# Kernel optimization log

Measured on AMD Instinct MI355X. Metric: run time of the kernel, lower is better.

## Reference

```python
import jax, jax.numpy as jnp
import numpy as np

B, L, DS, DP = 4, 384, 384, 128
NEAR_BAND = 4
LN_EPS = 1e-5


def setup_inputs():
    key = jax.random.key(0)
    k = jax.random.split(key, 16)
    return {
        "seq_repr": jax.random.normal(k[0], (B, L, DS), jnp.float32),
        "pair_repr": jax.random.normal(k[1], (B, L, L, DP), jnp.float32),
        "ln_s_g": 1.0 + 0.1 * jax.random.normal(k[2], (DS,), jnp.float32),
        "ln_s_b": 0.1 * jax.random.normal(k[3], (DS,), jnp.float32),
        "ln_z_g": 1.0 + 0.1 * jax.random.normal(k[4], (DP,), jnp.float32),
        "ln_z_b": 0.1 * jax.random.normal(k[5], (DP,), jnp.float32),
        "W_seq": jax.random.normal(k[6], (DS, DS), jnp.float32) / np.sqrt(DS).astype(np.float32),
        "W_pair": jax.random.normal(k[7], (DP, DP), jnp.float32) / np.sqrt(DP).astype(np.float32),
        "W_gs": 0.02 * jax.random.normal(k[8], (2 * DS, DS), jnp.float32),
        "b_gs": jnp.ones((DS,), jnp.float32),
        "W_gz": 0.02 * jax.random.normal(k[9], (2 * DP, DP), jnp.float32),
        "b_gz": jnp.ones((DP,), jnp.float32),
        "W1": jax.random.normal(k[10], (DS + 2 * DP, 64), jnp.float32) / np.sqrt(DS + 2 * DP).astype(np.float32),
        "b1": 0.01 * jax.random.normal(k[11], (64,), jnp.float32),
        "W2": jax.random.normal(k[12], (64, 1), jnp.float32) / 8.0,
        "b2": jnp.zeros((1,), jnp.float32),
        "chain_id": jax.random.randint(k[13], (B, L), 0, 2, jnp.int32),
        "mask": jax.random.randint(k[14], (B, L), 0, 2, jnp.int32).astype(jnp.bool_),
    }


def _layernorm(x, g, b):
    mu = jnp.mean(x, axis=-1, keepdims=True)
    var = jnp.mean(jnp.square(x - mu), axis=-1, keepdims=True)
    return (x - mu) * jax.lax.rsqrt(var + LN_EPS) * g + b


def _masked_mean(x, m, axes):
    num = jnp.sum(x * m, axis=axes)
    den = jnp.clip(jnp.sum(m, axis=axes), 1e-6, None)  # mask has trailing dim 1 -> den broadcasts
    return num / den


def _masked_max(x, m, axis):
    v = jnp.max(jnp.where(m > 0, x, -jnp.inf), axis=axis)
    return jnp.where(jnp.isinf(v), jnp.zeros_like(v), v)


def reference(seq_repr, pair_repr, ln_s_g, ln_s_b, ln_z_g, ln_z_b, W_seq, W_pair,
              W_gs, b_gs, W_gz, b_gz, W1, b1, W2, b2, chain_id, mask):
    # sequence branch: LN -> Linear -> masked mean/max over L -> gated blend
    s = _layernorm(seq_repr, ln_s_g, ln_s_b) @ W_seq          # [B,L,DS]
    m = mask.astype(s.dtype)[..., None]                        # [B,L,1]
    s_mean = _masked_mean(s, m, 1)                             # [B,DS]
    s_max = _masked_max(s, m, 1)                               # [B,DS]
    gate_s = jax.nn.sigmoid(jnp.concatenate([s_max, s_mean], -1) @ W_gs + b_gs)
    s_feat = s_mean + gate_s * (s_max - s_mean)

    # pair branch: symmetrize, zero diagonal, LN -> Linear
    p = 0.5 * (pair_repr + jnp.swapaxes(pair_repr, 1, 2))      # [B,L,L,DP]
    eye = jnp.eye(L, dtype=p.dtype)[None, :, :, None]
    p = p * (1.0 - eye)
    p = _layernorm(p, ln_z_g, ln_z_b) @ W_pair

    pm = (mask[:, :, None] & mask[:, None, :])[..., None].astype(p.dtype)   # [B,L,L,1]
    same = (chain_id[:, :, None] == chain_id[:, None, :])[..., None]
    intra = pm * same.astype(p.dtype)
    inter = pm * (~same).astype(p.dtype)

    inter_mean = _masked_mean(p, inter, (1, 2))                # [B,DP]
    row_den = jnp.clip(jnp.sum(inter, axis=2), 1e-6, None)     # [B,L,1]
    row_mean = jnp.sum(p * inter, axis=2) / row_den            # [B,L,DP]
    inter_peak = jnp.max(row_mean, axis=1)                     # [B,DP]
    gate_z = jax.nn.sigmoid(jnp.concatenate([inter_peak, inter_mean], -1) @ W_gz + b_gz)
    inter_feat = inter_mean + gate_z * (inter_peak - inter_mean)

    idx = jnp.arange(L)
    band = (jnp.abs(idx[:, None] - idx[None, :]) <= NEAR_BAND)[None, :, :, None].astype(p.dtype)
    intra_compact = _masked_mean(p, intra * band, (1, 2))      # [B,DP]

    feat = jnp.concatenate([s_feat, inter_feat, intra_compact], -1)  # [B, DS+2*DP]
    h = jax.nn.relu(feat @ W1 + b1)
    prob = jax.nn.sigmoid(h @ W2 + b2)[..., 0]                 # [B]
    return prob
```

## Files before the change

kernel.cpp:

```cpp
#include <hip/hip_runtime.h>
#include <hip/hip_bf16.h>
#include <math.h>

#define B_  4
#define L_  384
#define DS_ 384
#define DP_ 128
#define NB_ 4
#define FEAT_ (DS_ + 2*DP_)
#define LN_EPS_ 1e-5f
#define T_ 16
#define NT_ (L_ / T_)
#define NTP_ (NT_ * (NT_ + 1) / 2)
#define NCH_ 8
#define CHROWS_ (L_ / NCH_)

__device__ __forceinline__ void atomAddF(float* p, float v) {
    unsafeAtomicAdd(p, v);
}

__global__ __launch_bounds__(256) void k_mask(const void* __restrict__ mask_raw,
                                              int* __restrict__ maskN, int n) {
    const unsigned int* dw = (const unsigned int*)mask_raw;
    int tid = threadIdx.x;
    int local_int = 1, local_flt = 1;
    for (int i = tid; i < n / 4; i += blockDim.x) {
        unsigned int v = dw[i];
        if (v != 0u && v != 1u) local_int = 0;
        if (v != 0u && v != 0x3F800000u) local_flt = 0;
    }
    int all_int = __syncthreads_and(local_int);
    int all_flt = __syncthreads_and(local_flt);
    if (all_int) {
        for (int i = tid; i < n; i += blockDim.x) maskN[i] = (dw[i] != 0u) ? 1 : 0;
    } else if (all_flt) {
        const float* f = (const float*)mask_raw;
        for (int i = tid; i < n; i += blockDim.x) maskN[i] = (f[i] != 0.0f) ? 1 : 0;
    } else {
        const unsigned char* by = (const unsigned char*)mask_raw;
        for (int i = tid; i < n; i += blockDim.x) maskN[i] = by[i] ? 1 : 0;
    }
}

__global__ __launch_bounds__(256) void k_pair_tiles(
    const float* __restrict__ pair, const float* __restrict__ gz,
    const float* __restrict__ bz, const int* __restrict__ chain,
    const int* __restrict__ maskN,
    float* __restrict__ rs_inter, float* __restrict__ rs_intra,
    float* __restrict__ den_inter, float* __restrict__ den_intra) {
    extern __shared__ float lds[];
    float* smJI = lds;
    float* smJA = smJI + 4 * 16 * 128;
    float* smDJI = smJA + 4 * 16 * 128;
    float* smDJA = smDJI + 64;
    int* s_mi = (int*)(smDJA + 64);
    int* s_ci = s_mi + 16;
    int* s_mj = s_ci + 16;
    int* s_cj = s_mj + 16;

    const int b = blockIdx.x / NTP_;
    int t = blockIdx.x % NTP_;
    int ta = 0;
    while (t >= NT_ - ta) { t -= NT_ - ta; ta++; }
    const int tb = ta + t;
    const int i0 = ta * T_, j0 = tb * T_;
    const float fac = (ta == tb) ? 0.5f : 1.0f;

    const int tid = threadIdx.x;
    const int wave = tid >> 6, lane = tid & 63;
    const int ch2 = lane * 2;

    for (int idx = tid; idx < 4 * 16 * 128; idx += 256) { smJI[idx] = 0.f; smJA[idx] = 0.f; }
    if (tid < 64) { smDJI[tid] = 0.f; smDJA[tid] = 0.f; }
    if (tid < 16) {
        s_mi[tid] = maskN[b * L_ + i0 + tid];
        s_ci[tid] = chain[b * L_ + i0 + tid];
        s_mj[tid] = maskN[b * L_ + j0 + tid];
        s_cj[tid] = chain[b * L_ + j0 + tid];
    }
    __syncthreads();

    const float g0 = gz[ch2], g1 = gz[ch2 + 1];
    const float bb0 = bz[ch2], bb1 = bz[ch2 + 1];
    const float* baseb = pair + (size_t)b * L_ * L_ * DP_;

    float accI0[4] = {0, 0, 0, 0}, accI1[4] = {0, 0, 0, 0};
    float accA0[4] = {0, 0, 0, 0}, accA1[4] = {0, 0, 0, 0};
    float denI[4] = {0, 0, 0, 0}, denA[4] = {0, 0, 0, 0};

    for (int r = 0; r < 4; ++r) {
        const int il = (wave << 2) + r;
        const int gi = i0 + il;
        const int mi_ = s_mi[il];
        const int ci_ = s_ci[il];
        if (!mi_) continue;
        for (int jl = 0; jl < 16; ++jl) {
            const int gj = j0 + jl;
            if (!s_mj[jl]) continue;
            const bool same = (s_cj[jl] == ci_);
            int d = gi - gj; d = d < 0 ? -d : d;
            const float wI = (!same) ? fac : 0.f;
            const float wA = (same && d <= NB_) ? fac : 0.f;
            if (wI == 0.f && wA == 0.f) continue;
            float v0, v1;
            if (gi == gj) {
                v0 = 0.f; v1 = 0.f;
            } else {
                const float2 a = *(const float2*)(baseb + ((size_t)gi * L_ + gj) * DP_ + ch2);
                const float2 c = *(const float2*)(baseb + ((size_t)gj * L_ + gi) * DP_ + ch2);
                v0 = 0.5f * (a.x + c.x); v1 = 0.5f * (a.y + c.y);
            }
            float s = v0 + v1, q = v0 * v0 + v1 * v1;
            #pragma unroll
            for (int off = 32; off; off >>= 1) {
                s += __shfl_xor(s, off);
                q += __shfl_xor(q, off);
            }
            const float mu = s * (1.f / DP_);
            const float rstd = rsqrtf(q * (1.f / DP_) - mu * mu + LN_EPS_);
            const float y0 = (v0 - mu) * rstd * g0 + bb0;
            const float y1 = (v1 - mu) * rstd * g1 + bb1;
            accI0[r] += wI * y0; accI1[r] += wI * y1;
            accA0[r] += wA * y0; accA1[r] += wA * y1;
            denI[r] += wI; denA[r] += wA;
            float* pJI = smJI + ((wave * 16 + jl) << 7) + ch2;
            float* pJA = smJA + ((wave * 16 + jl) << 7) + ch2;
            pJI[0] += wI * y0; pJI[1] += wI * y1;
            pJA[0] += wA * y0; pJA[1] += wA * y1;
            if (lane == 0) { smDJI[wave * 16 + jl] += wI; smDJA[wave * 16 + jl] += wA; }
        }
    }
    __syncthreads();
    #pragma unroll
    for (int r = 0; r < 4; ++r) {
        const int gi = i0 + (wave << 2) + r;
        const size_t o = ((size_t)(b * L_ + gi) << 7) + ch2;
        atomAddF(&rs_inter[o], accI0[r]);
        atomAddF(&rs_inter[o + 1], accI1[r]);
        atomAddF(&rs_intra[o], accA0[r]);
        atomAddF(&rs_intra[o + 1], accA1[r]);
        if (lane == 0) {
            atomAddF(&den_inter[b * L_ + gi], denI[r]);
            atomAddF(&den_intra[b * L_ + gi], denA[r]);
        }
    }
    for (int idx = tid; idx < 16 * 128; idx += 256) {
        const int jl = idx >> 7, ch = idx & 127;
        const float vI = smJI[idx] + smJI[idx + 2048] + smJI[idx + 4096] + smJI[idx + 6144];
        const float vA = smJA[idx] + smJA[idx + 2048] + smJA[idx + 4096] + smJA[idx + 6144];
        const size_t o = ((size_t)(b * L_ + j0 + jl) << 7) + ch;
        atomAddF(&rs_inter[o], vI);
        atomAddF(&rs_intra[o], vA);
    }
    if (tid < 16) {
        const float dI = smDJI[tid] + smDJI[16 + tid] + smDJI[32 + tid] + smDJI[48 + tid];
        const float dA = smDJA[tid] + smDJA[16 + tid] + smDJA[32 + tid] + smDJA[48 + tid];
        atomAddF(&den_inter[b * L_ + j0 + tid], dI);
        atomAddF(&den_intra[b * L_ + j0 + tid], dA);
    }
}

#define SROWS_ 4
__global__ __launch_bounds__(384) void k_seq_proj(
    const float* __restrict__ seq, const float* __restrict__ gs,
    const float* __restrict__ bs, const float* __restrict__ W,
    float* __restrict__ s_rows) {
    const int row0 = blockIdx.x * SROWS_;
    const int tid = threadIdx.x;
    const int wave = tid >> 6, lane = tid & 63;
    __shared__ float xn[SROWS_][DS_];
    __shared__ float sSum[SROWS_][6], sSq[SROWS_][6];
    const float gg = gs[tid], bbv = bs[tid];
    #pragma unroll
    for (int r = 0; r < SROWS_; r++) {
        float x = seq[(size_t)(row0 + r) * DS_ + tid];
        float s = x, q = x * x;
        #pragma unroll
        for (int off = 32; off; off >>= 1) {
            s += __shfl_xor(s, off);
            q += __shfl_xor(q, off);
        }
        if (lane == 0) { sSum[r][wave] = s; sSq[r][wave] = q; }
        xn[r][tid] = x;
    }
    __syncthreads();
    float mu[SROWS_], rstd[SROWS_];
    #pragma unroll
    for (int r = 0; r < SROWS_; r++) {
        float ts = 0.f, tq = 0.f;
        #pragma unroll
        for (int w = 0; w < 6; w++) { ts += sSum[r][w]; tq += sSq[r][w]; }
        mu[r] = ts * (1.0f / DS_);
        float var = tq * (1.0f / DS_) - mu[r] * mu[r];
        rstd[r] = rsqrtf(var + LN_EPS_);
    }
    #pragma unroll
    for (int r = 0; r < SROWS_; r++)
        xn[r][tid] = (xn[r][tid] - mu[r]) * rstd[r] * gg + bbv;
    __syncthreads();
    float acc[SROWS_] = {0.f, 0.f, 0.f, 0.f};
    for (int k = 0; k < DS_; k++) {
        float w = W[(size_t)k * DS_ + tid];
        #pragma unroll
        for (int r = 0; r < SROWS_; r++) acc[r] += xn[r][k] * w;
    }
    #pragma unroll
    for (int r = 0; r < SROWS_; r++)
        s_rows[(size_t)(row0 + r) * DS_ + tid] = acc[r];
}

__global__ __launch_bounds__(384) void k_seq_partial(
    const float* __restrict__ s_rows, const int* __restrict__ maskN,
    float* __restrict__ psum, float* __restrict__ pmax, int* __restrict__ pcnt) {
    const int b = blockIdx.x / NCH_, c = blockIdx.x % NCH_;
    const int ch = threadIdx.x;
    float sum = 0.f, mx = -INFINITY;
    int cnt = 0;
    const int l0 = c * CHROWS_;
    for (int l = l0; l < l0 + CHROWS_; ++l) {
        if (maskN[b * L_ + l]) {
            float v = s_rows[(size_t)(b * L_ + l) * DS_ + ch];
            sum += v; mx = fmaxf(mx, v); cnt++;
        }
    }
    psum[(size_t)blockIdx.x * DS_ + ch] = sum;
    pmax[(size_t)blockIdx.x * DS_ + ch] = mx;
    if (ch == 0) pcnt[blockIdx.x] = cnt;
}

__global__ __launch_bounds__(128) void k_pair_partial(
    const float* __restrict__ rs_inter, const float* __restrict__ rs_intra,
    const float* __restrict__ den_inter, const float* __restrict__ den_intra,
    const float* __restrict__ Wp,
    float* __restrict__ pI, float* __restrict__ pA, float* __restrict__ pPk,
    float* __restrict__ pdI, float* __restrict__ pdA) {
    extern __shared__ float lds2[];
    float* sWp = lds2;
    float* sRS = sWp + 128 * 128;
    const int b = blockIdx.x / NCH_, c = blockIdx.x % NCH_;
    const int ch = threadIdx.x;
    for (int idx = ch; idx < 128 * 128; idx += 128) sWp[idx] = Wp[idx];
    float totI = 0.f, totA = 0.f, dI = 0.f, dA = 0.f, peak = -INFINITY;
    const int r0 = b * L_ + c * CHROWS_;
    for (int r = 0; r < CHROWS_; ++r) {
        __syncthreads();
        const float vI = rs_inter[(size_t)(r0 + r) * DP_ + ch];
        sRS[ch] = vI;
        totI += vI;
        totA += rs_intra[(size_t)(r0 + r) * DP_ + ch];
        const float den = den_inter[r0 + r];
        dI += den; dA += den_intra[r0 + r];
        __syncthreads();
        float acc = 0.f;
        for (int k = 0; k < 128; ++k) acc += sRS[k] * sWp[(k << 7) + ch];
        peak = fmaxf(peak, acc / fmaxf(den, 1e-6f));
    }
    pI[(size_t)blockIdx.x * DP_ + ch] = totI;
    pA[(size_t)blockIdx.x * DP_ + ch] = totA;
    pPk[(size_t)blockIdx.x * DP_ + ch] = peak;
    if (ch == 0) { pdI[blockIdx.x] = dI; pdA[blockIdx.x] = dA; }
}

__global__ __launch_bounds__(384) void k_finalize(
    const float* __restrict__ psum, const float* __restrict__ pmax,
    const int* __restrict__ pcnt,
    const float* __restrict__ pI, const float* __restrict__ pA,
    const float* __restrict__ pPk,
    const float* __restrict__ pdI, const float* __restrict__ pdA,
    const float* __restrict__ Wgs, const float* __restrict__ bgs,
    const float* __restrict__ Wp, const float* __restrict__ Wgz,
    const float* __restrict__ bgz,
    const float* __restrict__ W1, const float* __restrict__ b1,
    const float* __restrict__ W2, const float* __restrict__ b2,
    float* __restrict__ out) {
    const int b = blockIdx.x;
    const int tid = threadIdx.x;
    __shared__ float sMean[DS_], sMax[DS_], fI[DP_], fA[DP_], sPk[DP_], sIM[DP_];
    __shared__ float feat[FEAT_];
    __shared__ float sdI, sdA;
    {
        float s = 0.f, m = -INFINITY;
        int cnt = 0;
        for (int c = 0; c < NCH_; ++c) {
            s += psum[(size_t)(b * NCH_ + c) * DS_ + tid];
            m = fmaxf(m, pmax[(size_t)(b * NCH_ + c) * DS_ + tid]);
            cnt += pcnt[b * NCH_ + c];
        }
        sMean[tid] = s / fmaxf((float)cnt, 1e-6f);
        sMax[tid] = (cnt > 0) ? m : 0.f;
    }
    if (tid < DP_) {
        float tI = 0.f, tA = 0.f, pk = -INFINITY, ddI = 0.f, ddA = 0.f;
        for (int c = 0; c < NCH_; ++c) {
            tI += pI[(size_t)(b * NCH_ + c) * DP_ + tid];
            tA += pA[(size_t)(b * NCH_ + c) * DP_ + tid];
            pk = fmaxf(pk, pPk[(size_t)(b * NCH_ + c) * DP_ + tid]);
            ddI += pdI[b * NCH_ + c]; ddA += pdA[b * NCH_ + c];
        }
        fI[tid] = tI; fA[tid] = tA; sPk[tid] = pk;
        if (tid == 0) { sdI = ddI; sdA = ddA; }
    }
    __syncthreads();
    {
        float acc = bgs[tid];
        for (int k = 0; k < DS_; ++k)
            acc += sMax[k] * Wgs[(size_t)k * DS_ + tid]
                 + sMean[k] * Wgs[(size_t)(k + DS_) * DS_ + tid];
        const float gate = 1.f / (1.f + expf(-acc));
        feat[tid] = sMean[tid] + gate * (sMax[tid] - sMean[tid]);
    }
    if (tid < DP_) {
        float aI = 0.f, aA = 0.f;
        for (int k = 0; k < DP_; ++k) {
            aI += fI[k] * Wp[(k << 7) + tid];
            aA += fA[k] * Wp[(k << 7) + tid];
        }
        sIM[tid] = aI / fmaxf(sdI, 1e-6f);
        feat[DS_ + DP_ + tid] = aA / fmaxf(sdA, 1e-6f);
    }
    __syncthreads();
    if (tid < DP_) {
        float acc = bgz[tid];
        for (int k = 0; k < DP_; ++k)
            acc += sPk[k] * Wgz[(k << 7) + tid] + sIM[k] * Wgz[((k + DP_) << 7) + tid];
        const float gate = 1.f / (1.f + expf(-acc));
        feat[DS_ + tid] = sIM[tid] + gate * (sPk[tid] - sIM[tid]);
    }
    __syncthreads();
    if (tid < 64) {
        float acc = b1[tid];
        for (int k = 0; k < FEAT_; ++k) acc += feat[k] * W1[(k << 6) + tid];
        float p = fmaxf(acc, 0.f) * W2[tid];
        #pragma unroll
        for (int off = 32; off; off >>= 1) p += __shfl_xor(p, off);
        if (tid == 0) out[b] = 1.f / (1.f + expf(-(p + b2[0])));
    }
}

extern "C" void kernel_launch(void* const* d_in, const int* in_sizes, int n_in,
                              void* d_out, int out_size, void* d_ws, size_t ws_size,
                              hipStream_t stream) {
    const float* seq    = (const float*)d_in[0];
    const float* pair   = (const float*)d_in[1];
    const float* ln_s_g = (const float*)d_in[2];
    const float* ln_s_b = (const float*)d_in[3];
    const float* ln_z_g = (const float*)d_in[4];
    const float* ln_z_b = (const float*)d_in[5];
    const float* W_seq  = (const float*)d_in[6];
    const float* W_pair = (const float*)d_in[7];
    const float* W_gs   = (const float*)d_in[8];
    const float* b_gs   = (const float*)d_in[9];
    const float* W_gz   = (const float*)d_in[10];
    const float* b_gz   = (const float*)d_in[11];
    const float* W1     = (const float*)d_in[12];
    const float* b1     = (const float*)d_in[13];
    const float* W2     = (const float*)d_in[14];
    const float* b2     = (const float*)d_in[15];
    const int*   chain  = (const int*)d_in[16];
    const void*  mask   = d_in[17];
    float* out = (float*)d_out;

    char* ws = (char*)d_ws;
    float* rs_inter  = (float*)ws;  ws += (size_t)B_ * L_ * DP_ * 4;
    float* rs_intra  = (float*)ws;  ws += (size_t)B_ * L_ * DP_ * 4;
    float* den_inter = (float*)ws;  ws += (size_t)B_ * L_ * 4;
    float* den_intra = (float*)ws;  ws += (size_t)B_ * L_ * 4;
    const size_t zero_bytes = ((size_t)2 * B_ * L_ * DP_ + 2 * B_ * L_) * 4;
    int*   maskN = (int*)ws;        ws += (size_t)B_ * L_ * 4;
    float* s_rows = (float*)ws;     ws += (size_t)B_ * L_ * DS_ * 4;
    float* psum = (float*)ws;       ws += (size_t)B_ * NCH_ * DS_ * 4;
    float* pmax = (float*)ws;       ws += (size_t)B_ * NCH_ * DS_ * 4;
    int*   pcnt = (int*)ws;         ws += (size_t)B_ * NCH_ * 4;
    float* pI   = (float*)ws;       ws += (size_t)B_ * NCH_ * DP_ * 4;
    float* pA   = (float*)ws;       ws += (size_t)B_ * NCH_ * DP_ * 4;
    float* pPk  = (float*)ws;       ws += (size_t)B_ * NCH_ * DP_ * 4;
    float* pdI  = (float*)ws;       ws += (size_t)B_ * NCH_ * 4;
    float* pdA  = (float*)ws;       ws += (size_t)B_ * NCH_ * 4;

    const size_t ldsTiles = (size_t)(2 * 4 * 16 * 128 + 128 + 64) * 4;
    const size_t ldsPP    = (size_t)(128 * 128 + 128) * 4;

    hipMemsetAsync(rs_inter, 0, zero_bytes, stream);
    k_mask<<<1, 256, 0, stream>>>(mask, maskN, B_ * L_);
    k_pair_tiles<<<B_ * NTP_, 256, ldsTiles, stream>>>(
        pair, ln_z_g, ln_z_b, chain, maskN, rs_inter, rs_intra, den_inter, den_intra);
    k_seq_proj<<<(B_ * L_) / SROWS_, 384, 0, stream>>>(seq, ln_s_g, ln_s_b, W_seq, s_rows);
    k_seq_partial<<<B_ * NCH_, 384, 0, stream>>>(s_rows, maskN, psum, pmax, pcnt);
    k_pair_partial<<<B_ * NCH_, 128, ldsPP, stream>>>(
        rs_inter, rs_intra, den_inter, den_intra, W_pair, pI, pA, pPk, pdI, pdA);
    k_finalize<<<B_, 384, 0, stream>>>(psum, pmax, pcnt, pI, pA, pPk, pdI, pdA,
                                       W_gs, b_gs, W_pair, W_gz, b_gz,
                                       W1, b1, W2, b2, out);
}
```

Baseline: 685.0 us.

## Replace global atomics with per-tile partial buffers and fuse mask and reduction kernels

Pair tiles now write deterministic per-(tile,slot) partial row sums into a large workspace instead of atomically adding into global row sums. The memset and global atomics go away, and the per-wave LDS column accumulators become a single shared buffer updated with LDS atomics. Mask decoding is folded into each kernel, and the seq/pair partial-reduction kernels are merged into one launch with finer chunks. Pragma unrolls are added to the finalize loops. In exchange the code adds LDS atomic contention and extra global traffic to write and re-read the partial buffers.

```diff
diff --git a/kernel.cpp b/kernel.cpp
--- a/kernel.cpp
+++ b/kernel.cpp
@@ -1,5 +1,4 @@
 #include <hip/hip_runtime.h>
-#include <hip/hip_bf16.h>
 #include <math.h>
 
 #define B_  4
@@ -12,51 +11,44 @@
 #define T_ 16
 #define NT_ (L_ / T_)
 #define NTP_ (NT_ * (NT_ + 1) / 2)
-#define NCH_ 8
-#define CHROWS_ (L_ / NCH_)
-
-__device__ __forceinline__ void atomAddF(float* p, float v) {
-    unsafeAtomicAdd(p, v);
-}
-
-__global__ __launch_bounds__(256) void k_mask(const void* __restrict__ mask_raw,
-                                              int* __restrict__ maskN, int n) {
-    const unsigned int* dw = (const unsigned int*)mask_raw;
-    int tid = threadIdx.x;
-    int local_int = 1, local_flt = 1;
-    for (int i = tid; i < n / 4; i += blockDim.x) {
+#define SROWS_ 4
+
+__device__ __forceinline__ int detect_mode_block(const void* __restrict__ raw) {
+    const unsigned int* dw = (const unsigned int*)raw;
+    int li = 1, lf = 1;
+    for (int i = threadIdx.x; i < (B_ * L_) / 4; i += blockDim.x) {
         unsigned int v = dw[i];
-        if (v != 0u && v != 1u) local_int = 0;
-        if (v != 0u && v != 0x3F800000u) local_flt = 0;
-    }
-    int all_int = __syncthreads_and(local_int);
-    int all_flt = __syncthreads_and(local_flt);
-    if (all_int) {
-        for (int i = tid; i < n; i += blockDim.x) maskN[i] = (dw[i] != 0u) ? 1 : 0;
-    } else if (all_flt) {
-        const float* f = (const float*)mask_raw;
-        for (int i = tid; i < n; i += blockDim.x) maskN[i] = (f[i] != 0.0f) ? 1 : 0;
-    } else {
-        const unsigned char* by = (const unsigned char*)mask_raw;
-        for (int i = tid; i < n; i += blockDim.x) maskN[i] = by[i] ? 1 : 0;
-    }
+        if (v != 0u && v != 1u) li = 0;
+        if (v != 0u && v != 0x3F800000u) lf = 0;
+    }
+    int ai = __syncthreads_and(li);
+    int af = __syncthreads_and(lf);
+    return ai ? 0 : (af ? 1 : 2);
+}
+__device__ __forceinline__ int mask_at(const void* __restrict__ raw, int mode, int idx) {
+    if (mode == 0) return ((const unsigned int*)raw)[idx] != 0u;
+    if (mode == 1) return ((const float*)raw)[idx] != 0.0f;
+    return ((const unsigned char*)raw)[idx] != 0;
+}
+
+__device__ __forceinline__ size_t poff(int b, int tile, int slot, int row) {
+    return ((((size_t)b * NT_ + tile) * NT_ + slot) * T_ + row) * DP_;
+}
+__device__ __forceinline__ size_t pdoff(int b, int tile, int slot, int row) {
+    return (((size_t)b * NT_ + tile) * NT_ + slot) * T_ + row;
 }
 
 __global__ __launch_bounds__(256) void k_pair_tiles(
     const float* __restrict__ pair, const float* __restrict__ gz,
     const float* __restrict__ bz, const int* __restrict__ chain,
-    const int* __restrict__ maskN,
-    float* __restrict__ rs_inter, float* __restrict__ rs_intra,
-    float* __restrict__ den_inter, float* __restrict__ den_intra) {
-    extern __shared__ float lds[];
-    float* smJI = lds;
-    float* smJA = smJI + 4 * 16 * 128;
-    float* smDJI = smJA + 4 * 16 * 128;
-    float* smDJA = smDJI + 64;
-    int* s_mi = (int*)(smDJA + 64);
-    int* s_ci = s_mi + 16;
-    int* s_mj = s_ci + 16;
-    int* s_cj = s_mj + 16;
+    const void* __restrict__ mask_raw,
+    float* __restrict__ PI, float* __restrict__ PA,
+    float* __restrict__ PDI, float* __restrict__ PDA) {
+    __shared__ float smJI[T_][DP_], smJA[T_][DP_];
+    __shared__ float smDJI[T_], smDJA[T_];
+    __shared__ int s_m[2 * T_], s_c[2 * T_];
+
+    const int mode = detect_mode_block(mask_raw);
 
     const int b = blockIdx.x / NTP_;
     int t = blockIdx.x % NTP_;
@@ -70,13 +62,15 @@
     const int wave = tid >> 6, lane = tid & 63;
     const int ch2 = lane * 2;
 
-    for (int idx = tid; idx < 4 * 16 * 128; idx += 256) { smJI[idx] = 0.f; smJA[idx] = 0.f; }
-    if (tid < 64) { smDJI[tid] = 0.f; smDJA[tid] = 0.f; }
-    if (tid < 16) {
-        s_mi[tid] = maskN[b * L_ + i0 + tid];
-        s_ci[tid] = chain[b * L_ + i0 + tid];
-        s_mj[tid] = maskN[b * L_ + j0 + tid];
-        s_cj[tid] = chain[b * L_ + j0 + tid];
+    for (int idx = tid; idx < T_ * DP_; idx += 256) {
+        (&smJI[0][0])[idx] = 0.f;
+        (&smJA[0][0])[idx] = 0.f;
+    }
+    if (tid < T_) { smDJI[tid] = 0.f; smDJA[tid] = 0.f; }
+    if (tid < 2 * T_) {
+        const int loc = (tid < T_) ? (i0 + tid) : (j0 + tid - T_);
+        s_m[tid] = mask_at(mask_raw, mode, b * L_ + loc);
+        s_c[tid] = chain[b * L_ + loc];
     }
     __syncthreads();
 
@@ -91,13 +85,12 @@
     for (int r = 0; r < 4; ++r) {
         const int il = (wave << 2) + r;
         const int gi = i0 + il;
-        const int mi_ = s_mi[il];
-        const int ci_ = s_ci[il];
-        if (!mi_) continue;
-        for (int jl = 0; jl < 16; ++jl) {
+        if (!s_m[il]) continue;
+        const int ci = s_c[il];
+        for (int jl = 0; jl < T_; ++jl) {
+            if (!s_m[T_ + jl]) continue;
             const int gj = j0 + jl;
-            if (!s_mj[jl]) continue;
-            const bool same = (s_cj[jl] == ci_);
+            const bool same = (s_c[T_ + jl] == ci);
             int d = gi - gj; d = d < 0 ? -d : d;
             const float wI = (!same) ? fac : 0.f;
             const float wA = (same && d <= NB_) ? fac : 0.f;
@@ -123,44 +116,59 @@
             accI0[r] += wI * y0; accI1[r] += wI * y1;
             accA0[r] += wA * y0; accA1[r] += wA * y1;
             denI[r] += wI; denA[r] += wA;
-            float* pJI = smJI + ((wave * 16 + jl) << 7) + ch2;
-            float* pJA = smJA + ((wave * 16 + jl) << 7) + ch2;
-            pJI[0] += wI * y0; pJI[1] += wI * y1;
-            pJA[0] += wA * y0; pJA[1] += wA * y1;
-            if (lane == 0) { smDJI[wave * 16 + jl] += wI; smDJA[wave * 16 + jl] += wA; }
-        }
-    }
-    __syncthreads();
-    #pragma unroll
-    for (int r = 0; r < 4; ++r) {
-        const int gi = i0 + (wave << 2) + r;
-        const size_t o = ((size_t)(b * L_ + gi) << 7) + ch2;
-        atomAddF(&rs_inter[o], accI0[r]);
-        atomAddF(&rs_inter[o + 1], accI1[r]);
-        atomAddF(&rs_intra[o], accA0[r]);
-        atomAddF(&rs_intra[o + 1], accA1[r]);
-        if (lane == 0) {
-            atomAddF(&den_inter[b * L_ + gi], denI[r]);
-            atomAddF(&den_intra[b * L_ + gi], denA[r]);
-        }
-    }
-    for (int idx = tid; idx < 16 * 128; idx += 256) {
-        const int jl = idx >> 7, ch = idx & 127;
-        const float vI = smJI[idx] + smJI[idx + 2048] + smJI[idx + 4096] + smJI[idx + 6144];
-        const float vA = smJA[idx] + smJA[idx + 2048] + smJA[idx + 4096] + smJA[idx + 6144];
-        const size_t o = ((size_t)(b * L_ + j0 + jl) << 7) + ch;
-        atomAddF(&rs_inter[o], vI);
-        atomAddF(&rs_intra[o], vA);
-    }
-    if (tid < 16) {
-        const float dI = smDJI[tid] + smDJI[16 + tid] + smDJI[32 + tid] + smDJI[48 + tid];
-        const float dA = smDJA[tid] + smDJA[16 + tid] + smDJA[32 + tid] + smDJA[48 + tid];
-        atomAddF(&den_inter[b * L_ + j0 + tid], dI);
-        atomAddF(&den_intra[b * L_ + j0 + tid], dA);
-    }
-}
-
-#define SROWS_ 4
+            if (wI != 0.f) {
+                atomicAdd(&smJI[jl][ch2], wI * y0);
+                atomicAdd(&smJI[jl][ch2 + 1], wI * y1);
+                if (lane == 0) atomicAdd(&smDJI[jl], wI);
+            }
+            if (wA != 0.f) {
+                atomicAdd(&smJA[jl][ch2], wA * y0);
+                atomicAdd(&smJA[jl][ch2 + 1], wA * y1);
+                if (lane == 0) atomicAdd(&smDJA[jl], wA);
+            }
+        }
+    }
+    __syncthreads();
+
+    if (ta != tb) {
+        #pragma unroll
+        for (int r = 0; r < 4; ++r) {
+            const int il = (wave << 2) + r;
+            const size_t o = poff(b, ta, tb, il) + ch2;
+            PI[o] = accI0[r]; PI[o + 1] = accI1[r];
+            PA[o] = accA0[r]; PA[o + 1] = accA1[r];
+            if (lane == 0) {
+                PDI[pdoff(b, ta, tb, il)] = denI[r];
+                PDA[pdoff(b, ta, tb, il)] = denA[r];
+            }
+        }
+        for (int idx = tid; idx < T_ * DP_; idx += 256) {
+            const int jl = idx >> 7, ch = idx & 127;
+            const size_t o = poff(b, tb, ta, jl) + ch;
+            PI[o] = smJI[jl][ch];
+            PA[o] = smJA[jl][ch];
+        }
+        if (tid < T_) {
+            PDI[pdoff(b, tb, ta, tid)] = smDJI[tid];
+            PDA[pdoff(b, tb, ta, tid)] = smDJA[tid];
+        }
+    } else {
+        #pragma unroll
+        for (int r = 0; r < 4; ++r) {
+            const int il = (wave << 2) + r;
+            const size_t o = poff(b, ta, ta, il) + ch2;
+            PI[o] = accI0[r] + smJI[il][ch2];
+            PI[o + 1] = accI1[r] + smJI[il][ch2 + 1];
+            PA[o] = accA0[r] + smJA[il][ch2];
+            PA[o + 1] = accA1[r] + smJA[il][ch2 + 1];
+            if (lane == 0) {
+                PDI[pdoff(b, ta, ta, il)] = denI[r] + smDJI[il];
+                PDA[pdoff(b, ta, ta, il)] = denA[r] + smDJA[il];
+            }
+        }
+    }
+}
+
 __global__ __launch_bounds__(384) void k_seq_proj(
     const float* __restrict__ seq, const float* __restrict__ gs,
     const float* __restrict__ bs, const float* __restrict__ W,
@@ -209,56 +217,71 @@
         s_rows[(size_t)(row0 + r) * DS_ + tid] = acc[r];
 }
 
-__global__ __launch_bounds__(384) void k_seq_partial(
-    const float* __restrict__ s_rows, const int* __restrict__ maskN,
-    float* __restrict__ psum, float* __restrict__ pmax, int* __restrict__ pcnt) {
-    const int b = blockIdx.x / NCH_, c = blockIdx.x % NCH_;
-    const int ch = threadIdx.x;
-    float sum = 0.f, mx = -INFINITY;
-    int cnt = 0;
-    const int l0 = c * CHROWS_;
-    for (int l = l0; l < l0 + CHROWS_; ++l) {
-        if (maskN[b * L_ + l]) {
-            float v = s_rows[(size_t)(b * L_ + l) * DS_ + ch];
-            sum += v; mx = fmaxf(mx, v); cnt++;
-        }
-    }
-    psum[(size_t)blockIdx.x * DS_ + ch] = sum;
-    pmax[(size_t)blockIdx.x * DS_ + ch] = mx;
-    if (ch == 0) pcnt[blockIdx.x] = cnt;
-}
-
-__global__ __launch_bounds__(128) void k_pair_partial(
-    const float* __restrict__ rs_inter, const float* __restrict__ rs_intra,
-    const float* __restrict__ den_inter, const float* __restrict__ den_intra,
+__global__ __launch_bounds__(384) void k_mid(
+    const float* __restrict__ s_rows, const void* __restrict__ mask_raw,
     const float* __restrict__ Wp,
+    const float* __restrict__ PI, const float* __restrict__ PA,
+    const float* __restrict__ PDI, const float* __restrict__ PDA,
+    float* __restrict__ psum, float* __restrict__ pmax, int* __restrict__ pcnt,
     float* __restrict__ pI, float* __restrict__ pA, float* __restrict__ pPk,
     float* __restrict__ pdI, float* __restrict__ pdA) {
-    extern __shared__ float lds2[];
-    float* sWp = lds2;
-    float* sRS = sWp + 128 * 128;
-    const int b = blockIdx.x / NCH_, c = blockIdx.x % NCH_;
-    const int ch = threadIdx.x;
-    for (int idx = ch; idx < 128 * 128; idx += 128) sWp[idx] = Wp[idx];
-    float totI = 0.f, totA = 0.f, dI = 0.f, dA = 0.f, peak = -INFINITY;
-    const int r0 = b * L_ + c * CHROWS_;
-    for (int r = 0; r < CHROWS_; ++r) {
+    __shared__ float sWp[DP_ * DP_];
+    __shared__ float sRS[DP_];
+    const int tid = threadIdx.x;
+
+    if (blockIdx.x < B_ * NT_) {
+        const int b = blockIdx.x / NT_, tile = blockIdx.x % NT_;
+        for (int i = tid; i < DP_ * DP_; i += 384) sWp[i] = Wp[i];
         __syncthreads();
-        const float vI = rs_inter[(size_t)(r0 + r) * DP_ + ch];
-        sRS[ch] = vI;
-        totI += vI;
-        totA += rs_intra[(size_t)(r0 + r) * DP_ + ch];
-        const float den = den_inter[r0 + r];
-        dI += den; dA += den_intra[r0 + r];
-        __syncthreads();
-        float acc = 0.f;
-        for (int k = 0; k < 128; ++k) acc += sRS[k] * sWp[(k << 7) + ch];
-        peak = fmaxf(peak, acc / fmaxf(den, 1e-6f));
-    }
-    pI[(size_t)blockIdx.x * DP_ + ch] = totI;
-    pA[(size_t)blockIdx.x * DP_ + ch] = totA;
-    pPk[(size_t)blockIdx.x * DP_ + ch] = peak;
-    if (ch == 0) { pdI[blockIdx.x] = dI; pdA[blockIdx.x] = dA; }
+        float totI = 0.f, totA = 0.f, dI = 0.f, dA = 0.f, peak = -INFINITY;
+        for (int r = 0; r < T_; ++r) {
+            float dr = 0.f;
+            if (tid < DP_) {
+                float rsI = 0.f, rsA = 0.f, da = 0.f;
+                const size_t o0 = poff(b, tile, 0, r) + tid;
+                const size_t d0 = pdoff(b, tile, 0, r);
+                #pragma unroll 4
+                for (int s = 0; s < NT_; ++s) {
+                    rsI += PI[o0 + (size_t)s * T_ * DP_];
+                    rsA += PA[o0 + (size_t)s * T_ * DP_];
+                    dr += PDI[d0 + (size_t)s * T_];
+                    da += PDA[d0 + (size_t)s * T_];
+                }
+                sRS[tid] = rsI;
+                totI += rsI; totA += rsA; dI += dr; dA += da;
+            }
+            __syncthreads();
+            if (tid < DP_) {
+                float acc = 0.f;
+                #pragma unroll 8
+                for (int k = 0; k < DP_; ++k) acc += sRS[k] * sWp[(k << 7) + tid];
+                peak = fmaxf(peak, acc / fmaxf(dr, 1e-6f));
+            }
+            __syncthreads();
+        }
+        if (tid < DP_) {
+            pI[(size_t)(b * NT_ + tile) * DP_ + tid] = totI;
+            pA[(size_t)(b * NT_ + tile) * DP_ + tid] = totA;
+            pPk[(size_t)(b * NT_ + tile) * DP_ + tid] = peak;
+            if (tid == 0) { pdI[b * NT_ + tile] = dI; pdA[b * NT_ + tile] = dA; }
+        }
+    } else {
+        const int bi = blockIdx.x - B_ * NT_;
+        const int b = bi / NT_, tile = bi % NT_;
+        const int mode = detect_mode_block(mask_raw);
+        float sum = 0.f, mx = -INFINITY;
+        int cnt = 0;
+        const int l0 = tile * T_;
+        for (int l = l0; l < l0 + T_; ++l) {
+            if (mask_at(mask_raw, mode, b * L_ + l)) {
+                float v = s_rows[(size_t)(b * L_ + l) * DS_ + tid];
+                sum += v; mx = fmaxf(mx, v); cnt++;
+            }
+        }
+        psum[(size_t)(b * NT_ + tile) * DS_ + tid] = sum;
+        pmax[(size_t)(b * NT_ + tile) * DS_ + tid] = mx;
+        if (tid == 0) pcnt[b * NT_ + tile] = cnt;
+    }
 }
 
 __global__ __launch_bounds__(384) void k_finalize(
@@ -281,21 +304,21 @@
     {
         float s = 0.f, m = -INFINITY;
         int cnt = 0;
-        for (int c = 0; c < NCH_; ++c) {
-            s += psum[(size_t)(b * NCH_ + c) * DS_ + tid];
-            m = fmaxf(m, pmax[(size_t)(b * NCH_ + c) * DS_ + tid]);
-            cnt += pcnt[b * NCH_ + c];
+        for (int c = 0; c < NT_; ++c) {
+            s += psum[(size_t)(b * NT_ + c) * DS_ + tid];
+            m = fmaxf(m, pmax[(size_t)(b * NT_ + c) * DS_ + tid]);
+            cnt += pcnt[b * NT_ + c];
         }
         sMean[tid] = s / fmaxf((float)cnt, 1e-6f);
         sMax[tid] = (cnt > 0) ? m : 0.f;
     }
     if (tid < DP_) {
         float tI = 0.f, tA = 0.f, pk = -INFINITY, ddI = 0.f, ddA = 0.f;
-        for (int c = 0; c < NCH_; ++c) {
-            tI += pI[(size_t)(b * NCH_ + c) * DP_ + tid];
-            tA += pA[(size_t)(b * NCH_ + c) * DP_ + tid];
-            pk = fmaxf(pk, pPk[(size_t)(b * NCH_ + c) * DP_ + tid]);
-            ddI += pdI[b * NCH_ + c]; ddA += pdA[b * NCH_ + c];
+        for (int c = 0; c < NT_; ++c) {
+            tI += pI[(size_t)(b * NT_ + c) * DP_ + tid];
+            tA += pA[(size_t)(b * NT_ + c) * DP_ + tid];
+            pk = fmaxf(pk, pPk[(size_t)(b * NT_ + c) * DP_ + tid]);
+            ddI += pdI[b * NT_ + c]; ddA += pdA[b * NT_ + c];
         }
         fI[tid] = tI; fA[tid] = tA; sPk[tid] = pk;
         if (tid == 0) { sdI = ddI; sdA = ddA; }
@@ -303,6 +326,7 @@
     __syncthreads();
     {
         float acc = bgs[tid];
+        #pragma unroll 4
         for (int k = 0; k < DS_; ++k)
             acc += sMax[k] * Wgs[(size_t)k * DS_ + tid]
                  + sMean[k] * Wgs[(size_t)(k + DS_) * DS_ + tid];
@@ -311,6 +335,7 @@
     }
     if (tid < DP_) {
         float aI = 0.f, aA = 0.f;
+        #pragma unroll 4
         for (int k = 0; k < DP_; ++k) {
             aI += fI[k] * Wp[(k << 7) + tid];
             aA += fA[k] * Wp[(k << 7) + tid];
@@ -321,6 +346,7 @@
     __syncthreads();
     if (tid < DP_) {
         float acc = bgz[tid];
+        #pragma unroll 4
         for (int k = 0; k < DP_; ++k)
             acc += sPk[k] * Wgz[(k << 7) + tid] + sIM[k] * Wgz[((k + DP_) << 7) + tid];
         const float gate = 1.f / (1.f + expf(-acc));
@@ -329,6 +355,7 @@
     __syncthreads();
     if (tid < 64) {
         float acc = b1[tid];
+        #pragma unroll 4
         for (int k = 0; k < FEAT_; ++k) acc += feat[k] * W1[(k << 6) + tid];
         float p = fmaxf(acc, 0.f) * W2[tid];
         #pragma unroll
@@ -361,33 +388,27 @@
     float* out = (float*)d_out;
 
     char* ws = (char*)d_ws;
-    float* rs_inter  = (float*)ws;  ws += (size_t)B_ * L_ * DP_ * 4;
-    float* rs_intra  = (float*)ws;  ws += (size_t)B_ * L_ * DP_ * 4;
-    float* den_inter = (float*)ws;  ws += (size_t)B_ * L_ * 4;
-    float* den_intra = (float*)ws;  ws += (size_t)B_ * L_ * 4;
-    const size_t zero_bytes = ((size_t)2 * B_ * L_ * DP_ + 2 * B_ * L_) * 4;
-    int*   maskN = (int*)ws;        ws += (size_t)B_ * L_ * 4;
-    float* s_rows = (float*)ws;     ws += (size_t)B_ * L_ * DS_ * 4;
-    float* psum = (float*)ws;       ws += (size_t)B_ * NCH_ * DS_ * 4;
-    float* pmax = (float*)ws;       ws += (size_t)B_ * NCH_ * DS_ * 4;
-    int*   pcnt = (int*)ws;         ws += (size_t)B_ * NCH_ * 4;
-    float* pI   = (float*)ws;       ws += (size_t)B_ * NCH_ * DP_ * 4;
-    float* pA   = (float*)ws;       ws += (size_t)B_ * NCH_ * DP_ * 4;
-    float* pPk  = (float*)ws;       ws += (size_t)B_ * NCH_ * DP_ * 4;
-    float* pdI  = (float*)ws;       ws += (size_t)B_ * NCH_ * 4;
-    float* pdA  = (float*)ws;       ws += (size_t)B_ * NCH_ * 4;
-
-    const size_t ldsTiles = (size_t)(2 * 4 * 16 * 128 + 128 + 64) * 4;
-    const size_t ldsPP    = (size_t)(128 * 128 + 128) * 4;
-
-    hipMemsetAsync(rs_inter, 0, zero_bytes, stream);
-    k_mask<<<1, 256, 0, stream>>>(mask, maskN, B_ * L_);
-    k_pair_tiles<<<B_ * NTP_, 256, ldsTiles, stream>>>(
-        pair, ln_z_g, ln_z_b, chain, maskN, rs_inter, rs_intra, den_inter, den_intra);
+    const size_t nP  = (size_t)B_ * NT_ * NT_ * T_ * DP_;
+    const size_t nPD = (size_t)B_ * NT_ * NT_ * T_;
+    float* PI  = (float*)ws;  ws += nP * 4;
+    float* PA  = (float*)ws;  ws += nP * 4;
+    float* PDI = (float*)ws;  ws += nPD * 4;
+    float* PDA = (float*)ws;  ws += nPD * 4;
+    float* s_rows = (float*)ws; ws += (size_t)B_ * L_ * DS_ * 4;
+    float* psum = (float*)ws;   ws += (size_t)B_ * NT_ * DS_ * 4;
+    float* pmax = (float*)ws;   ws += (size_t)B_ * NT_ * DS_ * 4;
+    int*   pcnt = (int*)ws;     ws += (size_t)B_ * NT_ * 4;
+    float* pI   = (float*)ws;   ws += (size_t)B_ * NT_ * DP_ * 4;
+    float* pA   = (float*)ws;   ws += (size_t)B_ * NT_ * DP_ * 4;
+    float* pPk  = (float*)ws;   ws += (size_t)B_ * NT_ * DP_ * 4;
+    float* pdI  = (float*)ws;   ws += (size_t)B_ * NT_ * 4;
+    float* pdA  = (float*)ws;   ws += (size_t)B_ * NT_ * 4;
+
     k_seq_proj<<<(B_ * L_) / SROWS_, 384, 0, stream>>>(seq, ln_s_g, ln_s_b, W_seq, s_rows);
-    k_seq_partial<<<B_ * NCH_, 384, 0, stream>>>(s_rows, maskN, psum, pmax, pcnt);
-    k_pair_partial<<<B_ * NCH_, 128, ldsPP, stream>>>(
-        rs_inter, rs_intra, den_inter, den_intra, W_pair, pI, pA, pPk, pdI, pdA);
+    k_pair_tiles<<<B_ * NTP_, 256, 0, stream>>>(pair, ln_z_g, ln_z_b, chain, mask,
+                                                PI, PA, PDI, PDA);
+    k_mid<<<2 * B_ * NT_, 384, 0, stream>>>(s_rows, mask, W_pair, PI, PA, PDI, PDA,
+                                            psum, pmax, pcnt, pI, pA, pPk, pdI, pdA);
     k_finalize<<<B_, 384, 0, stream>>>(psum, pmax, pcnt, pI, pA, pPk, pdI, pdA,
                                        W_gs, b_gs, W_pair, W_gz, b_gz,
                                        W1, b1, W2, b2, out);
```

Measured after the change: 655.3 us. 1.05x faster.
